# Kernel optimization log

Hardware: AMD Instinct MI355X
Metric: run time of the kernel (lower is better)

The kernel has to match this reference:

```python
import jax, jax.numpy as jnp
import numpy as np

D_MODEL = 1024
N_HEADS = 16
D_HEAD = D_MODEL // N_HEADS          # 64
FRACTION_TO_ROTATE = 0.25
ROT_DIM = int(FRACTION_TO_ROTATE * D_HEAD)  # 16 (even)
ROPE_BASE = 10000.0


def setup_inputs() -> dict:
    key = jax.random.key(0)
    ks = jax.random.split(key, 10)
    B, S = 2, 2048
    init = lambda k, fan_in, shape: jax.random.normal(k, shape, jnp.float32) / np.sqrt(fan_in)
    return {
        "x": jax.random.normal(ks[0], (B, S, D_MODEL), jnp.float32),
        "Wq": init(ks[1], D_MODEL, (D_MODEL, D_MODEL)),
        "bq": jnp.zeros((D_MODEL,), jnp.float32),
        "Wk": init(ks[2], D_MODEL, (D_MODEL, D_MODEL)),
        "bk": jnp.zeros((D_MODEL,), jnp.float32),
        "Wv": init(ks[3], D_MODEL, (D_MODEL, D_MODEL)),
        "bv": jnp.zeros((D_MODEL,), jnp.float32),
        "Wo": init(ks[4], D_MODEL, (D_MODEL, D_MODEL)),
        "bo": jnp.zeros((D_MODEL,), jnp.float32),
    }


def _apply_partial_rope(t, cos, sin):
    # t: [B, H, S, d_head]; rotate first ROT_DIM dims, pass the rest through.
    rot, rest = t[..., :ROT_DIM], t[..., ROT_DIM:]
    half = ROT_DIM // 2
    t1, t2 = rot[..., :half], rot[..., half:]
    # cos/sin: [S, half] -> broadcast over [B, H]
    r1 = t1 * cos - t2 * sin
    r2 = t1 * sin + t2 * cos
    return jnp.concatenate([r1, r2, rest], axis=-1)


def reference(x, Wq, bq, Wk, bk, Wv, bv, Wo, bo):
    B, S, D = x.shape
    q = (x @ Wq + bq).reshape(B, S, N_HEADS, D_HEAD).transpose(0, 2, 1, 3)
    k = (x @ Wk + bk).reshape(B, S, N_HEADS, D_HEAD).transpose(0, 2, 1, 3)
    v = (x @ Wv + bv).reshape(B, S, N_HEADS, D_HEAD).transpose(0, 2, 1, 3)

    half = ROT_DIM // 2
    inv_freq = 1.0 / (ROPE_BASE ** (jnp.arange(half, dtype=jnp.float32) / half))
    angles = jnp.arange(S, dtype=jnp.float32)[:, None] * inv_freq  # [S, half]
    cos, sin = jnp.cos(angles), jnp.sin(angles)

    q = _apply_partial_rope(q, cos, sin)
    k = _apply_partial_rope(k, cos, sin)

    scale = 1.0 / np.sqrt(D_HEAD).astype(np.float32)
    scores = jnp.einsum("bhqd,bhkd->bhqk", q, k) * scale  # [B,H,S,S]
    causal = jnp.tril(jnp.ones((S, S), dtype=bool))
    scores = jnp.where(causal, scores, jnp.finfo(scores.dtype).min)
    probs = jax.nn.softmax(scores, axis=-1)

    out = jnp.einsum("bhqk,bhkd->bhqd", probs, v)  # [B,H,S,d_head]
    out = out.transpose(0, 2, 1, 3).reshape(B, S, D)
    return out @ Wo + bo
```

## Files before the change

kernel.cpp:

```cpp
#include <hip/hip_runtime.h>
#include <hip/hip_bf16.h>
#include <math.h>

constexpr int DM = 1024;
constexpr int SEQ = 2048;
constexpr int BATCH = 2;
constexpr int NH = 16;
constexpr int DH = 64;
constexpr int MROWS = BATCH * SEQ;
constexpr float SCALE = 0.125f;

typedef __attribute__((ext_vector_type(8))) short short8;
typedef __attribute__((ext_vector_type(4))) float f32x4;
typedef unsigned short ushort_t;

__device__ __forceinline__ unsigned short f2b(float f) {
    __hip_bfloat16 h = __float2bfloat16(f);
    return __builtin_bit_cast(unsigned short, h);
}
__device__ __forceinline__ float b2f(unsigned short u) {
    unsigned int t = ((unsigned int)u) << 16;
    return __builtin_bit_cast(float, t);
}
__device__ __forceinline__ unsigned int cvtpk_bf16(float lo, float hi) {
    unsigned int r;
    asm("v_cvt_pk_bf16_f32 %0, %1, %2" : "=v"(r) : "v"(lo), "v"(hi));
    return r;
}
__device__ __forceinline__ f32x4 mfma16_bf16(uint2 a, uint2 b, f32x4 c) {
    asm("v_mfma_f32_16x16x16_bf16 %0, %1, %2, %0"
        : "+v"(c) : "v"(a), "v"(b));
    return c;
}

__device__ __forceinline__ void gload16(const ushort_t* g, ushort_t* l) {
    __builtin_amdgcn_global_load_lds(
        (const __attribute__((address_space(1))) void*)g,
        (__attribute__((address_space(3))) void*)l, 16, 0, 0);
}

__global__ __launch_bounds__(256) void conv_x(const float* __restrict__ x,
                                              ushort_t* __restrict__ xb) {
    const size_t idx = (size_t)blockIdx.x * 256 + threadIdx.x;
    const float4* src = (const float4*)(x + idx * 8);
    float4 a = src[0], b = src[1];
    short8 v;
    v[0] = (short)f2b(a.x); v[1] = (short)f2b(a.y);
    v[2] = (short)f2b(a.z); v[3] = (short)f2b(a.w);
    v[4] = (short)f2b(b.x); v[5] = (short)f2b(b.y);
    v[6] = (short)f2b(b.z); v[7] = (short)f2b(b.w);
    *(short8*)(xb + idx * 8) = v;
}

__global__ __launch_bounds__(256) void conv_w(
    const float* __restrict__ Wq, const float* __restrict__ Wk,
    const float* __restrict__ Wv, const float* __restrict__ Wo,
    ushort_t* __restrict__ Wqt, ushort_t* __restrict__ Wkt,
    ushort_t* __restrict__ Wvt, ushort_t* __restrict__ Wot) {
    const float* W; ushort_t* Wt;
    switch (blockIdx.z) {
        case 0:  W = Wq; Wt = Wqt; break;
        case 1:  W = Wk; Wt = Wkt; break;
        case 2:  W = Wv; Wt = Wvt; break;
        default: W = Wo; Wt = Wot; break;
    }
    __shared__ float L[64][65];
    const int n0 = blockIdx.x * 64, k0 = blockIdx.y * 64;
    const int t = threadIdx.x;
    const int tr = t >> 4, tc4 = (t & 15) * 4;
#pragma unroll
    for (int i = 0; i < 4; ++i) {
        int kk = tr + i * 16;
        float4 v = *(const float4*)&W[(size_t)(k0 + kk) * DM + n0 + tc4];
        L[kk][tc4 + 0] = v.x; L[kk][tc4 + 1] = v.y;
        L[kk][tc4 + 2] = v.z; L[kk][tc4 + 3] = v.w;
    }
    __syncthreads();
#pragma unroll
    for (int i = 0; i < 4; ++i) {
        int nn = tr + i * 16;
        ushort4 u;
        u.x = f2b(L[tc4 + 0][nn]); u.y = f2b(L[tc4 + 1][nn]);
        u.z = f2b(L[tc4 + 2][nn]); u.w = f2b(L[tc4 + 3][nn]);
        *(ushort4*)&Wt[(size_t)(n0 + nn) * DM + k0 + tc4] = u;
    }
}

#define BM 128
#define BN 128
#define BKK 32
#define NKT (DM / BKK)

__device__ __forceinline__ void stage_tile(const ushort_t* __restrict__ A,
                                           const ushort_t* __restrict__ B,
                                           int row0, int col0, int kt,
                                           ushort_t* As, ushort_t* Bs, int tid) {
#pragma unroll
    for (int i = 0; i < 2; ++i) {
        int f = i * 256 + tid;
        int r = f >> 2, c = (f & 3) ^ (r & 3);
        gload16(&A[(size_t)(row0 + r) * DM + kt * BKK + c * 8], &As[f * 8]);
        gload16(&B[(size_t)(col0 + r) * DM + kt * BKK + c * 8], &Bs[f * 8]);
    }
}

__device__ __forceinline__ void mfma_core(const ushort_t* __restrict__ A,
                                          const ushort_t* __restrict__ B,
                                          int row0, int col0,
                                          ushort_t* smem, f32x4 (&acc)[4][4]) {
    const int tid = threadIdx.x;
    const int wave = tid >> 6, lane = tid & 63;
    const int lg = lane >> 4, ln = lane & 15;
    const int wr = wave >> 1, wc = wave & 1;

    stage_tile(A, B, row0, col0, 0, smem, smem + 4096, tid);
    __syncthreads();

    int cur = 0;
    for (int kt = 0; kt < NKT; ++kt) {
        ushort_t* As = smem + cur * 8192;
        ushort_t* Bs = As + 4096;
        if (kt + 1 < NKT) {
            ushort_t* An = smem + (cur ^ 1) * 8192;
            stage_tile(A, B, row0, col0, kt + 1, An, An + 4096, tid);
        }

        short8 af[4], bf[4];
#pragma unroll
        for (int mi = 0; mi < 4; ++mi) {
            int r = wr * 64 + mi * 16 + ln;
            af[mi] = *(const short8*)&As[r * 32 + ((lg ^ (r & 3)) * 8)];
        }
#pragma unroll
        for (int ni = 0; ni < 4; ++ni) {
            int r = wc * 64 + ni * 16 + ln;
            bf[ni] = *(const short8*)&Bs[r * 32 + ((lg ^ (r & 3)) * 8)];
        }
        __builtin_amdgcn_s_setprio(1);
#pragma unroll
        for (int mi = 0; mi < 4; ++mi)
#pragma unroll
            for (int ni = 0; ni < 4; ++ni)
                acc[mi][ni] = __builtin_amdgcn_mfma_f32_16x16x32_bf16(
                    af[mi], bf[ni], acc[mi][ni], 0, 0, 0);
        __builtin_amdgcn_s_setprio(0);

        __syncthreads();
        cur ^= 1;
    }
}

__global__ __launch_bounds__(256) void mfma_gemm_qkv(
    const ushort_t* __restrict__ xb,
    const ushort_t* __restrict__ Wqt, const ushort_t* __restrict__ Wkt,
    const ushort_t* __restrict__ Wvt,
    const float* __restrict__ bq, const float* __restrict__ bk,
    const float* __restrict__ bv,
    ushort_t* __restrict__ qb, ushort_t* __restrict__ kb,
    ushort_t* __restrict__ vtb) {
    const ushort_t* W; const float* bias;
    if (blockIdx.z == 0)      { W = Wqt; bias = bq; }
    else if (blockIdx.z == 1) { W = Wkt; bias = bk; }
    else                      { W = Wvt; bias = bv; }

    const int row0 = blockIdx.y * BM;
    const int col0 = blockIdx.x * BN;
    __shared__ ushort_t smem[16384];
    f32x4 acc[4][4] = {};
    mfma_core(xb, W, row0, col0, smem, acc);

    const int tid = threadIdx.x;
    const int wave = tid >> 6, lane = tid & 63;
    const int lg = lane >> 4, ln = lane & 15;
    const int wr = wave >> 1, wc = wave & 1;
    const bool isV = (blockIdx.z == 2);

    __syncthreads();
    ushort_t* Cs = smem;
#pragma unroll
    for (int mi = 0; mi < 4; ++mi)
#pragma unroll
        for (int ni = 0; ni < 4; ++ni)
#pragma unroll
            for (int r = 0; r < 4; ++r) {
                int mrel = wr * 64 + mi * 16 + lg * 4 + r;
                int nrel = wc * 64 + ni * 16 + ln;
                float v = acc[mi][ni][r] + bias[col0 + nrel];
                Cs[isV ? (nrel * 128 + mrel) : (mrel * 128 + nrel)] = f2b(v);
            }
    __syncthreads();

    if (!isV) {
        ushort_t* out = (blockIdx.z == 0) ? qb : kb;
#pragma unroll
        for (int i = 0; i < 8; ++i) {
            int f = i * 256 + tid;
            int rrow = f >> 4, c8 = f & 15;
            int m = row0 + rrow;
            int b = m >> 11, s = m & (SEQ - 1);
            int n = col0 + c8 * 8;
            int h = n >> 6, d = n & 63;
            short8 val;
            if (d < 16) {
                const ushort_t* base = &Cs[rrow * 128 + (c8 & 8) * 8];
                const bool hi = (d >= 8);
#pragma unroll
                for (int j = 0; j < 8; ++j) {
                    float t1 = b2f(base[j]);
                    float t2 = b2f(base[8 + j]);
                    float invf = __expf(-(float)j * 1.1512925465f);
                    float ang = (float)s * invf;
                    float c_, si_;
                    __sincosf(ang, &si_, &c_);
                    val[j] = (short)f2b(hi ? (t1 * si_ + t2 * c_)
                                           : (t1 * c_ - t2 * si_));
                }
            } else {
                val = *(const short8*)&Cs[rrow * 128 + c8 * 8];
            }
            *(short8*)&out[((size_t)((b * NH + h) * SEQ) + s) * DH + d] = val;
        }
    } else {
#pragma unroll
        for (int i = 0; i < 8; ++i) {
            int f = i * 256 + tid;
            int nrow = f >> 4, c8 = f & 15;
            int n = col0 + nrow;
            int h = n >> 6, d = n & 63;
            int m = row0 + c8 * 8;
            int b = m >> 11, s = m & (SEQ - 1);
            *(short8*)&vtb[((size_t)((b * NH + h) * DH) + d) * SEQ + s] =
                *(const short8*)&Cs[nrow * 128 + c8 * 8];
        }
    }
}

__global__ __launch_bounds__(256) void mfma_gemm_out(
    const ushort_t* __restrict__ ctxb, const ushort_t* __restrict__ Wot,
    const float* __restrict__ bo, float* __restrict__ out) {
    const int row0 = blockIdx.y * BM;
    const int col0 = blockIdx.x * BN;
    __shared__ ushort_t smem[16384];
    f32x4 acc[4][4] = {};
    mfma_core(ctxb, Wot, row0, col0, smem, acc);

    const int tid = threadIdx.x;
    const int wave = tid >> 6, lane = tid & 63;
    const int lg = lane >> 4, ln = lane & 15;
    const int wr = wave >> 1, wc = wave & 1;
#pragma unroll
    for (int mi = 0; mi < 4; ++mi)
#pragma unroll
        for (int ni = 0; ni < 4; ++ni)
#pragma unroll
            for (int r = 0; r < 4; ++r) {
                int m = row0 + wr * 64 + mi * 16 + lg * 4 + r;
                int n = col0 + wc * 64 + ni * 16 + ln;
                out[(size_t)m * DM + n] = acc[mi][ni][r] + bo[n];
            }
}

#define AQT 64
#define AKT 64
#define NQT (SEQ / AQT)

__global__ __launch_bounds__(256) void attn_mfma(
    const ushort_t* __restrict__ qb, const ushort_t* __restrict__ kb,
    const ushort_t* __restrict__ vtb, ushort_t* __restrict__ ctxb,
    ushort_t* __restrict__ opart, float* __restrict__ lpart) {
    constexpr float C1 = 0.18033688f;
    constexpr float M2 = 1.44269504f;
    const int bh = blockIdx.x;
    const int y = blockIdx.y;

    int qt, t0, t1, chunk;
    if (y < 16)      { qt = 16 + y;  t0 = 0;  t1 = 16;     chunk = 0; }
    else if (y < 32) { qt = 47 - y;  t0 = 16; t1 = qt + 1; chunk = 1; }
    else             { qt = 47 - y;  t0 = 0;  t1 = qt + 1; chunk = -1; }
    const int q0 = qt * AQT;

    const int tid = threadIdx.x;
    const int wave = tid >> 6;
    const int lane = tid & 63;
    const int lg = lane >> 4;
    const int ln = lane & 15;

    __shared__ ushort_t KT[2][64 * 64];
    __shared__ ushort_t VT[2][64 * 64];

    const ushort_t* kbase = kb + (size_t)bh * SEQ * DH;
    const ushort_t* vbase = vtb + (size_t)bh * DH * SEQ;
    const int b = bh >> 4, h = bh & 15;

    const ushort_t* qrow = qb + ((size_t)bh * SEQ + q0 + wave * 16 + ln) * DH;
    short8 qf0 = *(const short8*)&qrow[lg * 8];
    short8 qf1 = *(const short8*)&qrow[32 + lg * 8];

    f32x4 o[4];
#pragma unroll
    for (int nt = 0; nt < 4; nt++) o[nt] = f32x4{0.f, 0.f, 0.f, 0.f};
    float l = 0.f;

#pragma unroll
    for (int i = 0; i < 2; i++) {
        int f = i * 256 + tid;
        int r = f >> 3, p = f & 7, c = p ^ (r & 7);
        gload16(&kbase[(size_t)(t0 * AKT + r) * DH + c * 8], &KT[0][f * 8]);
        gload16(&vbase[(size_t)r * SEQ + t0 * AKT + c * 8], &VT[0][f * 8]);
    }

    int cur = 0;
    for (int t = t0; t < t1; ++t) {
        __syncthreads();

        if (t + 1 < t1) {
            const int nb0 = (t + 1) * AKT;
            const int nxt = cur ^ 1;
#pragma unroll
            for (int i = 0; i < 2; i++) {
                int f = i * 256 + tid;
                int r = f >> 3, p = f & 7, c = p ^ (r & 7);
                gload16(&kbase[(size_t)(nb0 + r) * DH + c * 8], &KT[nxt][f * 8]);
                gload16(&vbase[(size_t)r * SEQ + nb0 + c * 8], &VT[nxt][f * 8]);
            }
        }

        float st[4][4];
        __builtin_amdgcn_s_setprio(1);
#pragma unroll
        for (int kt = 0; kt < 4; kt++) {
            f32x4 acc = f32x4{0.f, 0.f, 0.f, 0.f};
            int krow = kt * 16 + ln;
            short8 b0 = *(const short8*)&KT[cur][krow * 64 + ((lg ^ (krow & 7)) * 8)];
            short8 b1 = *(const short8*)&KT[cur][krow * 64 + (((4 + lg) ^ (krow & 7)) * 8)];
            acc = __builtin_amdgcn_mfma_f32_16x16x32_bf16(b0, qf0, acc, 0, 0, 0);
            acc = __builtin_amdgcn_mfma_f32_16x16x32_bf16(b1, qf1, acc, 0, 0, 0);
#pragma unroll
            for (int r = 0; r < 4; r++) st[kt][r] = acc[r];
        }
        __builtin_amdgcn_s_setprio(0);

        if (t == qt) {
            const int qrel = wave * 16 + ln;
#pragma unroll
            for (int kt = 0; kt < 4; kt++)
#pragma unroll
                for (int r = 0; r < 4; r++)
                    if (kt * 16 + lg * 4 + r > qrel) st[kt][r] = -1e30f;
        }

        uint2 pkq[4];
#pragma unroll
        for (int kt = 0; kt < 4; kt++) {
            float pv[4];
#pragma unroll
            for (int r = 0; r < 4; r++) {
                pv[r] = exp2f(fmaf(C1, st[kt][r], -M2));
                l += pv[r];
            }
            pkq[kt].x = cvtpk_bf16(pv[0], pv[1]);
            pkq[kt].y = cvtpk_bf16(pv[2], pv[3]);
        }

        __builtin_amdgcn_s_setprio(1);
#pragma unroll
        for (int nt = 0; nt < 4; nt++) {
            int vrow = nt * 16 + ln;
#pragma unroll
            for (int kt = 0; kt < 4; kt++) {
                int chunk16 = (2 * kt + (lg >> 1)) ^ (vrow & 7);
                uint2 vb = *(const uint2*)&VT[cur][vrow * 64 + chunk16 * 8 + (lg & 1) * 4];
                o[nt] = mfma16_bf16(pkq[kt], vb, o[nt]);
            }
        }
        __builtin_amdgcn_s_setprio(0);

        cur ^= 1;
    }

    l += __shfl_xor(l, 16);
    l += __shfl_xor(l, 32);

    if (chunk >= 0) {
        const int pid = ((bh << 4) + (qt - 16)) * 2 + chunk;
        if (lg == 0) lpart[pid * 64 + wave * 16 + ln] = l;
        ushort_t* ob = opart + (size_t)pid * 4096;
#pragma unroll
        for (int r = 0; r < 4; r++) {
            int qrel = wave * 16 + lg * 4 + r;
#pragma unroll
            for (int nt = 0; nt < 4; nt++)
                ob[qrel * 64 + nt * 16 + ln] = f2b(o[nt][r]);
        }
    } else {
        const float rcp = 1.f / l;
#pragma unroll
        for (int r = 0; r < 4; r++) {
            float invl = __shfl(rcp, (lane & 48) | (lg * 4 + r));
            int qg = q0 + wave * 16 + lg * 4 + r;
            ushort_t* op = ctxb + ((size_t)(b * SEQ + qg)) * DM + h * DH;
#pragma unroll
            for (int nt = 0; nt < 4; nt++)
                op[nt * 16 + ln] = f2b(o[nt][r] * invl);
        }
    }
}

__global__ __launch_bounds__(256) void attn_reduce(
    const ushort_t* __restrict__ opart, const float* __restrict__ lpart,
    ushort_t* __restrict__ ctxb) {
    const int bh = blockIdx.x;
    const int qt = 16 + blockIdx.y;
    const int tid = threadIdx.x;
    const int q = tid >> 2;
    const int d0 = (tid & 3) * 16;

    const int pid0 = ((bh << 4) + (qt - 16)) * 2;
    const ushort_t* o0 = opart + (size_t)pid0 * 4096 + q * 64 + d0;
    const ushort_t* o1 = opart + (size_t)(pid0 + 1) * 4096 + q * 64 + d0;
    const float inv = 1.f / (lpart[pid0 * 64 + q] + lpart[(pid0 + 1) * 64 + q]);

    const int b = bh >> 4, h = bh & 15;
    ushort_t* op = ctxb + ((size_t)(b * SEQ + qt * 64 + q)) * DM + h * DH + d0;
#pragma unroll
    for (int half = 0; half < 2; ++half) {
        short8 a = *(const short8*)&o0[half * 8];
        short8 c = *(const short8*)&o1[half * 8];
        short8 r;
#pragma unroll
        for (int j = 0; j < 8; ++j)
            r[j] = (short)f2b((b2f((unsigned short)a[j]) +
                               b2f((unsigned short)c[j])) * inv);
        *(short8*)&op[half * 8] = r;
    }
}

extern "C" void kernel_launch(void* const* d_in, const int* in_sizes, int n_in,
                              void* d_out, int out_size, void* d_ws, size_t ws_size,
                              hipStream_t stream) {
    const float* x  = (const float*)d_in[0];
    const float* Wq = (const float*)d_in[1];
    const float* bq = (const float*)d_in[2];
    const float* Wk = (const float*)d_in[3];
    const float* bk = (const float*)d_in[4];
    const float* Wv = (const float*)d_in[5];
    const float* bv = (const float*)d_in[6];
    const float* Wo = (const float*)d_in[7];
    const float* bo = (const float*)d_in[8];
    float* out = (float*)d_out;

    constexpr size_t TSZ = (size_t)MROWS * DM;
    constexpr size_t WSZ = (size_t)DM * DM;
    ushort_t* xb  = (ushort_t*)d_ws;
    ushort_t* Wqt = xb + TSZ;
    ushort_t* Wkt = Wqt + WSZ;
    ushort_t* Wvt = Wkt + WSZ;
    ushort_t* Wot = Wvt + WSZ;
    ushort_t* qbp = Wot + WSZ;
    ushort_t* kbp = qbp + TSZ;
    ushort_t* vtp = kbp + TSZ;
    ushort_t* ctxb = vtp + TSZ;

    ushort_t* opart = xb;
    float* lpart = (float*)Wqt;

    conv_x<<<TSZ / 8 / 256, 256, 0, stream>>>(x, xb);
    conv_w<<<dim3(16, 16, 4), 256, 0, stream>>>(Wq, Wk, Wv, Wo, Wqt, Wkt, Wvt, Wot);

    mfma_gemm_qkv<<<dim3(DM / BN, MROWS / BM, 3), 256, 0, stream>>>(
        xb, Wqt, Wkt, Wvt, bq, bk, bv, qbp, kbp, vtp);

    attn_mfma<<<dim3(BATCH * NH, 48), 256, 0, stream>>>(
        qbp, kbp, vtp, ctxb, opart, lpart);
    attn_reduce<<<dim3(BATCH * NH, 16), 256, 0, stream>>>(opart, lpart, ctxb);

    mfma_gemm_out<<<dim3(DM / BN, MROWS / BM), 256, 0, stream>>>(ctxb, Wot, bo, out);
}
```

Before: 117.5 us.

## Triple-buffer GEMM LDS tiles with vmcnt waits and new XOR swizzle

Moves the shared GEMM core from double to triple buffering. It prefetches two k-tiles ahead and waits with explicit vmcnt counts plus one barrier per iteration, instead of two __syncthreads. The LDS layout is re-swizzled so two rows share a 128-byte line with an XOR over 8 chunks, aiming to cut bank conflicts on the 16-byte MFMA fragment reads. LDS use per block grows from 32 KB to 48 KB, which may limit occupancy. The single-barrier scheme also depends on the vmcnt accounting matching the async load count.

```diff
diff --git a/kernel.cpp b/kernel.cpp
--- a/kernel.cpp
+++ b/kernel.cpp
@@ -98,7 +98,10 @@
 #pragma unroll
     for (int i = 0; i < 2; ++i) {
         int f = i * 256 + tid;
-        int r = f >> 2, c = (f & 3) ^ (r & 3);
+        int sr = f >> 3, p = f & 7;
+        int u = p ^ (sr & 7);
+        int r = 2 * sr + (u >> 2);
+        int c = u & 3;
         gload16(&A[(size_t)(row0 + r) * DM + kt * BKK + c * 8], &As[f * 8]);
         gload16(&B[(size_t)(col0 + r) * DM + kt * BKK + c * 8], &Bs[f * 8]);
     }
@@ -114,27 +117,37 @@
     const int wr = wave >> 1, wc = wave & 1;
 
     stage_tile(A, B, row0, col0, 0, smem, smem + 4096, tid);
-    __syncthreads();
-
-    int cur = 0;
+    __builtin_amdgcn_sched_barrier(0);
+    stage_tile(A, B, row0, col0, 1, smem + 8192, smem + 12288, tid);
+
     for (int kt = 0; kt < NKT; ++kt) {
-        ushort_t* As = smem + cur * 8192;
-        ushort_t* Bs = As + 4096;
-        if (kt + 1 < NKT) {
-            ushort_t* An = smem + (cur ^ 1) * 8192;
-            stage_tile(A, B, row0, col0, kt + 1, An, An + 4096, tid);
-        }
-
+        if (kt + 1 < NKT)
+            asm volatile("s_waitcnt vmcnt(4)" ::: "memory");
+        else
+            asm volatile("s_waitcnt vmcnt(0)" ::: "memory");
+        __builtin_amdgcn_s_barrier();
+
+        if (kt + 2 < NKT) {
+            ushort_t* An = smem + ((kt + 2) % 3) * 8192;
+            stage_tile(A, B, row0, col0, kt + 2, An, An + 4096, tid);
+        }
+
+        const ushort_t* As = smem + (kt % 3) * 8192;
+        const ushort_t* Bs = As + 4096;
         short8 af[4], bf[4];
 #pragma unroll
         for (int mi = 0; mi < 4; ++mi) {
             int r = wr * 64 + mi * 16 + ln;
-            af[mi] = *(const short8*)&As[r * 32 + ((lg ^ (r & 3)) * 8)];
+            int sr = r >> 1;
+            int p = (((r & 1) << 2) | lg) ^ (sr & 7);
+            af[mi] = *(const short8*)&As[sr * 64 + p * 8];
         }
 #pragma unroll
         for (int ni = 0; ni < 4; ++ni) {
             int r = wc * 64 + ni * 16 + ln;
-            bf[ni] = *(const short8*)&Bs[r * 32 + ((lg ^ (r & 3)) * 8)];
+            int sr = r >> 1;
+            int p = (((r & 1) << 2) | lg) ^ (sr & 7);
+            bf[ni] = *(const short8*)&Bs[sr * 64 + p * 8];
         }
         __builtin_amdgcn_s_setprio(1);
 #pragma unroll
@@ -144,9 +157,6 @@
                 acc[mi][ni] = __builtin_amdgcn_mfma_f32_16x16x32_bf16(
                     af[mi], bf[ni], acc[mi][ni], 0, 0, 0);
         __builtin_amdgcn_s_setprio(0);
-
-        __syncthreads();
-        cur ^= 1;
     }
 }
 
@@ -165,7 +175,7 @@
 
     const int row0 = blockIdx.y * BM;
     const int col0 = blockIdx.x * BN;
-    __shared__ ushort_t smem[16384];
+    __shared__ ushort_t smem[24576];
     f32x4 acc[4][4] = {};
     mfma_core(xb, W, row0, col0, smem, acc);
 
@@ -240,7 +250,7 @@
     const float* __restrict__ bo, float* __restrict__ out) {
     const int row0 = blockIdx.y * BM;
     const int col0 = blockIdx.x * BN;
-    __shared__ ushort_t smem[16384];
+    __shared__ ushort_t smem[24576];
     f32x4 acc[4][4] = {};
     mfma_core(ctxb, Wot, row0, col0, smem, acc);
 
```

Result: no change. 116.3 us (-1.0%).
